# Kernel optimization log

Measured on AMD Instinct MI355X. Metric: run time of the kernel, lower is better.

## Reference

```python
import jax, jax.numpy as jnp
import numpy as np

WINDOW = 129  # must be odd; matches init_kwargs


def setup_inputs() -> dict:
    key = jax.random.key(0)
    kq, kk, kv = jax.random.split(key, 3)
    shape = (1, 2048, 8, 64)  # (b, s, nh, h)
    return {
        "q": jax.random.normal(kq, shape, dtype=jnp.float32),
        "k": jax.random.normal(kk, shape, dtype=jnp.float32),
        "v": jax.random.normal(kv, shape, dtype=jnp.float32),
    }


def reference(q, k, v):
    # Sliding-window local attention, faithful to the pad+unfold torch module.
    b, s, nh, h = k.shape
    w = (WINDOW - 1) // 2
    W = 2 * w + 1
    scale = h ** (-0.5)
    qn = q * scale

    # zero-pad keys/values along the sequence dim by w on both sides
    kp = jnp.pad(k, ((0, 0), (w, w), (0, 0), (0, 0)))  # (b, s+2w, nh, h)
    vp = jnp.pad(v, ((0, 0), (w, w), (0, 0), (0, 0)))

    # idx[j, q] = j + q : padded key position for window offset j at query q
    idx = jnp.arange(W)[:, None] + jnp.arange(s)[None, :]  # (W, s)
    kw = kp[:, idx]  # (b, W, s, nh, h) -- unfolded key windows
    vw = vp[:, idx]  # (b, W, s, nh, h)

    # A[b, q, j, n] = <q[b,q,n,:], k_padded[b, j+q, n, :]>
    A = jnp.einsum('bqnh,bjqnh->bqjn', qn, kw)

    # mask out window slots pointing at padding (key pos j+q-w outside [0, s))
    valid = (idx >= w) & (idx < s + w)  # (W, s)
    mask_value = -jnp.finfo(A.dtype).max
    A = jnp.where(valid.T[None, :, :, None], A, mask_value)  # (1, s, W, 1) bcast

    # softmax over the window-offset axis (dim=-2 in the torch module)
    A = jax.nn.softmax(A, axis=2)

    # z[b, q, n, h] = sum_j A[b,q,j,n] * v_padded[b, j+q, n, h]
    z = jnp.einsum('bqjn,bjqnh->bqnh', A, vw)
    return z
```

## Files before the change

kernel.cpp:

```cpp
#include <hip/hip_runtime.h>
#include <math.h>


typedef __attribute__((ext_vector_type(8))) short short8;
typedef __attribute__((ext_vector_type(4))) float f32x4;

namespace {
constexpr int SEQ = 2048, NH = 8, HD = 64, WHALF = 64;
constexpr int TQ  = 16;
constexpr int ROWS = 144;
constexpr int KST  = 72;
constexpr int PST  = 184;
constexpr int NHD  = NH * HD;
}

__device__ __forceinline__ ushort f2bf(float x) {
  return (ushort)((__float_as_uint(x) + 0x8000u) >> 16);
}
__device__ __forceinline__ float fexp2(float x) {
  float r;
  asm("v_exp_f32 %0, %1" : "=v"(r) : "v"(x));
  return r;
}
__device__ __forceinline__ float frcp(float x) {
  float r;
  asm("v_rcp_f32 %0, %1" : "=v"(r) : "v"(x));
  return r;
}

__global__ __launch_bounds__(256, 4) void wattn_kernel(
    const float* __restrict__ q, const float* __restrict__ k,
    const float* __restrict__ v, float* __restrict__ out) {
  __shared__ __align__(16) short sK[ROWS * KST];
  __shared__ __align__(16) short sQ[TQ * KST];
  __shared__ __align__(16) short sP[TQ * PST];
  __shared__ __align__(16) float sD[64];

  const int t = threadIdx.x;
  const int bid  = blockIdx.x + (int)gridDim.x * blockIdx.y;
  const int W    = (bid & 7) * 128 + (bid >> 3);
  const int tile = W & 127;
  const int n    = W >> 7;
  const int q0   = tile * TQ;
  const size_t hb = (size_t)n * HD;

  const int w = t >> 6, lane = t & 63, lq = lane & 15, lg = lane >> 4;

  if (t < 64) {
    int qq = t >> 2, r0 = ROWS + 4 * (t & 3);
    *(uint2*)&sP[qq * PST + r0] = make_uint2(0u, 0u);
  }

  #pragma unroll
  for (int it = 0; it < 9; ++it) {
    int f = t + it * 256;
    int row = f >> 4, c16 = f & 15;
    int grow = q0 - WHALF + row;
    int cg = min(max(grow, 0), SEQ - 1);
    float4 kv = *(const float4*)(k + (size_t)cg * NHD + hb + c16 * 4);
    uint lo = (uint)f2bf(kv.x) | ((uint)f2bf(kv.y) << 16);
    uint hi = (uint)f2bf(kv.z) | ((uint)f2bf(kv.w) << 16);
    *(uint2*)&sK[row * KST + c16 * 4] = make_uint2(lo, hi);
  }
  {
    int row = t >> 4, c16 = t & 15;
    float4 qv = *(const float4*)(q + (size_t)(q0 + row) * NHD + hb + c16 * 4);
    uint lo = (uint)f2bf(qv.x) | ((uint)f2bf(qv.y) << 16);
    uint hi = (uint)f2bf(qv.z) | ((uint)f2bf(qv.w) << 16);
    *(uint2*)&sQ[row * KST + c16 * 4] = make_uint2(lo, hi);
  }

  const float* vcol = v + hb + w * 16 + lq;
  float vf[5][8];
  #pragma unroll
  for (int kc = 0; kc < 5; ++kc)
    #pragma unroll
    for (int j = 0; j < 8; ++j) {
      int row  = kc * 32 + 8 * lg + j;
      int grow = q0 - WHALF + row;
      int cg   = min(max(grow, 0), SEQ - 1);
      vf[kc][j] = vcol[(size_t)cg * NHD];
    }

  __syncthreads();

  const short8 qf0 = *(const short8*)&sQ[lq * KST + 8 * lg];
  const short8 qf1 = *(const short8*)&sQ[lq * KST + 32 + 8 * lg];

  const float EXPC = 0.125f * 1.4426950408889634f;

  auto do_tile = [&](int rb, float& ws) {
    short8 kf0 = *(const short8*)&sK[(rb + lq) * KST + 8 * lg];
    short8 kf1 = *(const short8*)&sK[(rb + lq) * KST + 32 + 8 * lg];
    f32x4 acc = {0.f, 0.f, 0.f, 0.f};
    acc = __builtin_amdgcn_mfma_f32_16x16x32_bf16(kf0, qf0, acc, 0, 0, 0);
    acc = __builtin_amdgcn_mfma_f32_16x16x32_bf16(kf1, qf1, acc, 0, 0, 0);
    ushort pb[4];
    #pragma unroll
    for (int r = 0; r < 4; ++r) {
      int row = rb + 4 * lg + r;
      int g2  = q0 - WHALF + row;
      bool valid = (row >= lq) && (row <= lq + 2 * WHALF) && (g2 >= 0) && (g2 < SEQ);
      float p = valid ? fexp2((float)acc[r] * EXPC) : 0.f;
      ws += p;
      pb[r] = f2bf(p);
    }
    uint lo = (uint)pb[0] | ((uint)pb[1] << 16);
    uint hi = (uint)pb[2] | ((uint)pb[3] << 16);
    *(uint2*)&sP[lq * PST + rb + 4 * lg] = make_uint2(lo, hi);
  };

  float ws = 0.f;
  do_tile(w * 16, ws);
  do_tile((w + 4) * 16, ws);
  if (w == 0) do_tile(8 * 16, ws);

  ws += __shfl_xor(ws, 16);
  ws += __shfl_xor(ws, 32);
  if (lane < 16) sD[w * 16 + lane] = ws;

  __syncthreads();

  float4 dsum = make_float4(0.f, 0.f, 0.f, 0.f);
  #pragma unroll
  for (int w2 = 0; w2 < 4; ++w2) {
    float4 dp = *(const float4*)(sD + w2 * 16 + 4 * lg);
    dsum.x += dp.x; dsum.y += dp.y; dsum.z += dp.z; dsum.w += dp.w;
  }
  short8 pa[5];
  #pragma unroll
  for (int kc = 0; kc < 5; ++kc)
    pa[kc] = *(const short8*)&sP[lq * PST + kc * 32 + 8 * lg];

  f32x4 acc = {0.f, 0.f, 0.f, 0.f};
  #pragma unroll
  for (int kc = 0; kc < 5; ++kc) {
    short8 vb;
    #pragma unroll
    for (int j = 0; j < 8; ++j) vb[j] = (short)f2bf(vf[kc][j]);
    acc = __builtin_amdgcn_mfma_f32_16x16x32_bf16(pa[kc], vb, acc, 0, 0, 0);
  }

  float di[4] = {frcp(dsum.x), frcp(dsum.y), frcp(dsum.z), frcp(dsum.w)};
  float* op = out + (size_t)(q0 + 4 * lg) * NHD + hb + w * 16 + lq;
  #pragma unroll
  for (int r = 0; r < 4; ++r)
    op[(size_t)r * NHD] = (float)acc[r] * di[r];
}

extern "C" void kernel_launch(void* const* d_in, const int* in_sizes, int n_in,
                              void* d_out, int out_size, void* d_ws, size_t ws_size,
                              hipStream_t stream) {
  const float* q = (const float*)d_in[0];
  const float* k = (const float*)d_in[1];
  const float* v = (const float*)d_in[2];
  float* out = (float*)d_out;
  dim3 grid(SEQ / TQ, NH);
  hipLaunchKernelGGL(wattn_kernel, grid, dim3(256), 0, stream, q, k, v, out);
}
```

Measured before the change: 12.04 us.

## Double query tile to 32 rows with 512-thread blocks to cut K/V halo reloads

Each block now handles 32 queries instead of 16, using 8 waves that split into query halves and head-dim quarters. The staged K/V window grows from 144 to 160 rows, so the redundant halo rows loaded and converted per query drop noticeably. Validity masking is simplified to precomputed per-query row bounds, and all P tiles are now written directly, so the explicit zero-padding of sP is no longer needed. In exchange the grid is halved to 512 blocks, which may reduce latency hiding on a GPU with many CUs.

```diff
diff --git a/kernel.cpp b/kernel.cpp
--- a/kernel.cpp
+++ b/kernel.cpp
@@ -7,10 +7,10 @@
 
 namespace {
 constexpr int SEQ = 2048, NH = 8, HD = 64, WHALF = 64;
-constexpr int TQ  = 16;
-constexpr int ROWS = 144;
+constexpr int TQ  = 32;
+constexpr int ROWS = 160;
 constexpr int KST  = 72;
-constexpr int PST  = 184;
+constexpr int PST  = 168;
 constexpr int NHD  = NH * HD;
 }
 
@@ -28,32 +28,29 @@
   return r;
 }
 
-__global__ __launch_bounds__(256, 4) void wattn_kernel(
+__global__ __launch_bounds__(512, 4) void wattn_kernel(
     const float* __restrict__ q, const float* __restrict__ k,
     const float* __restrict__ v, float* __restrict__ out) {
   __shared__ __align__(16) short sK[ROWS * KST];
   __shared__ __align__(16) short sQ[TQ * KST];
   __shared__ __align__(16) short sP[TQ * PST];
-  __shared__ __align__(16) float sD[64];
+  __shared__ __align__(16) float sD[8 * 16];
 
   const int t = threadIdx.x;
-  const int bid  = blockIdx.x + (int)gridDim.x * blockIdx.y;
-  const int W    = (bid & 7) * 128 + (bid >> 3);
-  const int tile = W & 127;
-  const int n    = W >> 7;
+  const int bid  = blockIdx.x;
+  const int W    = (bid & 7) * 64 + (bid >> 3);
+  const int tile = W & 63;
+  const int n    = W >> 6;
   const int q0   = tile * TQ;
   const size_t hb = (size_t)n * HD;
 
   const int w = t >> 6, lane = t & 63, lq = lane & 15, lg = lane >> 4;
-
-  if (t < 64) {
-    int qq = t >> 2, r0 = ROWS + 4 * (t & 3);
-    *(uint2*)&sP[qq * PST + r0] = make_uint2(0u, 0u);
-  }
+  const int qh = w & 1;
+  const int ht = w >> 1;
 
   #pragma unroll
-  for (int it = 0; it < 9; ++it) {
-    int f = t + it * 256;
+  for (int it = 0; it < 5; ++it) {
+    int f = t + it * 512;
     int row = f >> 4, c16 = f & 15;
     int grow = q0 - WHALF + row;
     int cg = min(max(grow, 0), SEQ - 1);
@@ -70,7 +67,7 @@
     *(uint2*)&sQ[row * KST + c16 * 4] = make_uint2(lo, hi);
   }
 
-  const float* vcol = v + hb + w * 16 + lq;
+  const float* vcol = v + hb + ht * 16 + lq;
   float vf[5][8];
   #pragma unroll
   for (int kc = 0; kc < 5; ++kc)
@@ -84,12 +81,16 @@
 
   __syncthreads();
 
-  const short8 qf0 = *(const short8*)&sQ[lq * KST + 8 * lg];
-  const short8 qf1 = *(const short8*)&sQ[lq * KST + 32 + 8 * lg];
+  const int qd = qh * 16 + lq;
+  const short8 qf0 = *(const short8*)&sQ[qd * KST + 8 * lg];
+  const short8 qf1 = *(const short8*)&sQ[qd * KST + 32 + 8 * lg];
 
   const float EXPC = 0.125f * 1.4426950408889634f;
+  const int rlo = max(qd, WHALF - q0);
+  const int rhi = min(qd + 2 * WHALF, SEQ - 1 + WHALF - q0);
 
-  auto do_tile = [&](int rb, float& ws) {
+  auto do_tile = [&](int rt, float& ws) {
+    const int rb = rt * 16;
     short8 kf0 = *(const short8*)&sK[(rb + lq) * KST + 8 * lg];
     short8 kf1 = *(const short8*)&sK[(rb + lq) * KST + 32 + 8 * lg];
     f32x4 acc = {0.f, 0.f, 0.f, 0.f};
@@ -99,21 +100,20 @@
     #pragma unroll
     for (int r = 0; r < 4; ++r) {
       int row = rb + 4 * lg + r;
-      int g2  = q0 - WHALF + row;
-      bool valid = (row >= lq) && (row <= lq + 2 * WHALF) && (g2 >= 0) && (g2 < SEQ);
+      bool valid = (row >= rlo) && (row <= rhi);
       float p = valid ? fexp2((float)acc[r] * EXPC) : 0.f;
       ws += p;
       pb[r] = f2bf(p);
     }
     uint lo = (uint)pb[0] | ((uint)pb[1] << 16);
     uint hi = (uint)pb[2] | ((uint)pb[3] << 16);
-    *(uint2*)&sP[lq * PST + rb + 4 * lg] = make_uint2(lo, hi);
+    *(uint2*)&sP[qd * PST + rb + 4 * lg] = make_uint2(lo, hi);
   };
 
   float ws = 0.f;
-  do_tile(w * 16, ws);
-  do_tile((w + 4) * 16, ws);
-  if (w == 0) do_tile(8 * 16, ws);
+  do_tile(ht, ws);
+  do_tile(ht + 4, ws);
+  if (w < 4) do_tile(8 + (w >> 1), ws);
 
   ws += __shfl_xor(ws, 16);
   ws += __shfl_xor(ws, 32);
@@ -123,14 +123,14 @@
 
   float4 dsum = make_float4(0.f, 0.f, 0.f, 0.f);
   #pragma unroll
-  for (int w2 = 0; w2 < 4; ++w2) {
-    float4 dp = *(const float4*)(sD + w2 * 16 + 4 * lg);
+  for (int j = 0; j < 4; ++j) {
+    float4 dp = *(const float4*)(sD + (qh + 2 * j) * 16 + 4 * lg);
     dsum.x += dp.x; dsum.y += dp.y; dsum.z += dp.z; dsum.w += dp.w;
   }
   short8 pa[5];
   #pragma unroll
   for (int kc = 0; kc < 5; ++kc)
-    pa[kc] = *(const short8*)&sP[lq * PST + kc * 32 + 8 * lg];
+    pa[kc] = *(const short8*)&sP[qd * PST + kc * 32 + 8 * lg];
 
   f32x4 acc = {0.f, 0.f, 0.f, 0.f};
   #pragma unroll
@@ -142,7 +142,7 @@
   }
 
   float di[4] = {frcp(dsum.x), frcp(dsum.y), frcp(dsum.z), frcp(dsum.w)};
-  float* op = out + (size_t)(q0 + 4 * lg) * NHD + hb + w * 16 + lq;
+  float* op = out + (size_t)(q0 + qh * 16 + 4 * lg) * NHD + hb + ht * 16 + lq;
   #pragma unroll
   for (int r = 0; r < 4; ++r)
     op[(size_t)r * NHD] = (float)acc[r] * di[r];
@@ -155,6 +155,6 @@
   const float* k = (const float*)d_in[1];
   const float* v = (const float*)d_in[2];
   float* out = (float*)d_out;
-  dim3 grid(SEQ / TQ, NH);
-  hipLaunchKernelGGL(wattn_kernel, grid, dim3(256), 0, stream, q, k, v, out);
+  dim3 grid((SEQ / TQ) * NH);
+  hipLaunchKernelGGL(wattn_kernel, grid, dim3(512), 0, stream, q, k, v, out);
 }
```

Measured after the change: 10.77 us. -10.6%, faster.
